# Kernel optimization log

Measured on AMD Instinct MI355X. Metric: run time of the kernel, lower is better.

Reference implementation:

```python
import jax, jax.numpy as jnp
import numpy as np

K = 3
THETA0 = 0.5
THETA1 = 30.0
ALPHA0 = 3.0
BASE = 0.45
ITERS = 20


def unfold(x, k):
    # torch.nn.Unfold(k, stride=1, padding=k//2): [N,C,H,W] -> [N,C,k*k,H*W]
    # kernel positions in row-major (ki,kj) order, zero padding (matches torch)
    p = k // 2
    N, C, H, W = x.shape
    xp = jnp.pad(x, ((0, 0), (0, 0), (p, p), (p, p)))
    patches = jnp.stack([xp[:, :, i:i + H, j:j + W]
                         for i in range(k) for j in range(k)], axis=2)
    return patches.reshape(N, C, k * k, H * W)


def setup_inputs() -> dict:
    key = jax.random.key(0)
    k1, k2, k3 = jax.random.split(key, 3)
    B, C, H, W = 4, 3, 384, 384
    x = jax.random.uniform(k1, (B, 1, H, W), dtype=jnp.float32)
    targets = jax.random.uniform(k2, (B, 1, H, W), dtype=jnp.float32)
    feature_map = jax.random.uniform(k3, (B, C, H, W), dtype=jnp.float32)
    return {"x": x, "targets": targets, "feature_map": feature_map}


def reference(x, targets, feature_map):
    B, C, H, W = feature_map.shape
    HW = H * W

    # ---- precompute pairwise kernel (done in __init__ in torch) ----
    fm = feature_map + 10.0
    ufm = unfold(fm, K)                                  # [B,C,k2,HW]
    ar = np.arange(K * K)
    spatial = jnp.asarray(((ar // K - K // 2) ** 2 +
                           (ar % K - K // 2) ** 2), dtype=jnp.float32)
    color = -jnp.sum((ufm - fm.reshape(B, C, 1, HW)) ** 2, axis=1) / (2.0 * THETA0 ** 2)
    kernel = ALPHA0 * jnp.exp(color - spatial.reshape(1, -1, 1) / (2.0 * THETA1 ** 2))  # [B,k2,HW]

    # ---- forward ----
    xm = x * targets
    xm = (xm > 0.5).astype(x.dtype) * (1.0 - 2.0 * BASE) + BASE
    ret = jnp.concatenate([1.0 - xm, xm], axis=1)        # [B,2,H,W]

    def body(_, r):
        u = unfold(-jnp.log(r), K)                       # [B,2,k2,HW]
        aggre = jnp.sum(u * kernel[:, None], axis=2)     # [B,2,HW]
        f = jnp.exp(-aggre).reshape(B, 2, H, W)
        f = jnp.concatenate([f[:, :1], f[:, 1:] * targets], axis=1)
        f = f + 1e-6
        f = f / jnp.sum(f, axis=1, keepdims=True)
        f = (f > 0.5).astype(f.dtype) * (1.0 - 2.0 * BASE) + BASE
        return f

    ret = jax.lax.fori_loop(0, ITERS, body, ret)

    out = (ret[:, 1:] > 0.5).astype(ret.dtype)           # [B,1,H,W]
    count = jnp.sum(out.reshape(B, -1), axis=1)
    valid = ((count >= HW * 0.05) & (count <= HW * 0.95)).astype(jnp.float32)
    return out, valid
```

## Files before the change

kernel.cpp:

```cpp
#include <hip/hip_runtime.h>
#include <math.h>

namespace {

constexpr int Hh = 384;
constexpr int Ww = 384;
constexpr int Bb = 4;
constexpr int HW = Hh * Ww;
constexpr int NPIX = Bb * HW;
constexpr int ROUNDS = 10;
constexpr int TPB = 256;

constexpr int TILE_W = 64;
constexpr int TILE_H = 8;
constexpr int TX = Ww / TILE_W;
constexpr int TY = Hh / TILE_H;
constexpr int BLKS_PER_B = TX * TY;
constexpr int NBLK = Bb * BLKS_PER_B;

constexpr int H2DW = 20;
constexpr int H2TOT = 12 * H2DW;

constexpr int MIDS = 68;
constexpr int NRING = 148;

constexpr int FMR = 12, FMC = 70, FMPL = FMR * FMC;
constexpr int FMTOT = 3 * FMPL;
constexpr int QR = 11, QC = 68, QPL = QR * QC;
constexpr int QTOT = 4 * QPL;

__device__ __forceinline__ float fsub_rn_(float a, float b) {
    return __fadd_rn(a, -b);
}

__device__ __forceinline__ unsigned ld_agent_u32(const void* p) {
    return __hip_atomic_load((const unsigned*)p, __ATOMIC_RELAXED,
                             __HIP_MEMORY_SCOPE_AGENT);
}
__device__ __forceinline__ void st_agent_u16(void* p, unsigned short v) {
    __hip_atomic_store((unsigned short*)p, v, __ATOMIC_RELAXED,
                       __HIP_MEMORY_SCOPE_AGENT);
}
__device__ __forceinline__ int ld_agent_i32(const int* p) {
    return __hip_atomic_load(p, __ATOMIC_RELAXED, __HIP_MEMORY_SCOPE_AGENT);
}
__device__ __forceinline__ void st_agent_i32(int* p, int v) {
    __hip_atomic_store(p, v, __ATOMIC_RELAXED, __HIP_MEMORY_SCOPE_AGENT);
}

template <int STRIDE>
__device__ __forceinline__ unsigned mf_state(const unsigned char* base,
                                             const float* w9, float tpx,
                                             float Lg45, float Lg55) {
    float a0 = 0.0f, a1 = 0.0f;
#pragma unroll
    for (int ki = 0; ki < 3; ++ki) {
#pragma unroll
        for (int kj = 0; kj < 3; ++kj) {
            const int k = ki * 3 + kj;
            unsigned char s = base[ki * STRIDE + kj];
            float u0 = (s & 1) ? Lg55 : Lg45;
            float u1 = (s & 2) ? Lg55 : Lg45;
            a0 = __fadd_rn(a0, __fmul_rn(u0, w9[k]));
            a1 = __fadd_rn(a1, __fmul_rn(u1, w9[k]));
        }
    }
    float f0 = expf(-a0);
    float f1 = __fmul_rn(expf(-a1), tpx);
    f0 = __fadd_rn(f0, 1e-6f);
    f1 = __fadd_rn(f1, 1e-6f);
    float S = __fadd_rn(f0, f1);
    float f0n = __fdiv_rn(f0, S);
    float f1n = __fdiv_rn(f1, S);
    return (f0n > 0.5f ? 1u : 0u) | (f1n > 0.5f ? 2u : 0u);
}

__device__ __forceinline__ void ring_coords(int ri, int& er, int& ec) {
    if (ri < 66)       { er = 0;        ec = ri; }
    else if (ri < 132) { er = 9;        ec = ri - 66; }
    else if (ri < 140) { er = ri - 131; ec = 0; }
    else               { er = ri - 139; ec = 65; }
}

__global__ __launch_bounds__(TPB, 6) void fused_kernel(
        const float* __restrict__ x, const float* __restrict__ t,
        const float* __restrict__ fm, float* __restrict__ out,
        int* __restrict__ arrive, int* __restrict__ flags,
        int* __restrict__ partial,
        unsigned char* __restrict__ st0, unsigned char* __restrict__ st1) {
    const int tid = threadIdx.x;
    const int bid = blockIdx.x;
    const int b = bid / BLKS_PER_B;
    const int rr_ = bid - b * BLKS_PER_B;
    const int ty = rr_ / TX, tx = rr_ - ty * TX;
    const int row0 = ty * TILE_H, col0 = tx * TILE_W;
    const int tr = tid >> 5;
    const int tc = (tid & 31) * 2;
    const int row = row0 + tr, col = col0 + tc;
    const int hw = row * Ww + col;
    const int gp = b * HW + hw;

    bool nactive = false;
    const int* nflag = nullptr;
    if (tid < 8) {
        const int l2 = (tid < 4) ? tid : tid + 1;
        const int dy = l2 / 3 - 1, dx = l2 - (l2 / 3) * 3 - 1;
        const int nty = ty + dy, ntx = tx + dx;
        if (nty >= 0 && nty < TY && ntx >= 0 && ntx < TX) {
            nactive = true;
            nflag = &flags[(b * BLKS_PER_B + nty * TX + ntx) << 4];
        }
    }

    const float Lg45 = (float)(-log((double)0.45f));
    const float Lg55 = (float)(-log((double)0.55f));

    float2 xv = reinterpret_cast<const float2*>(x)[gp >> 1];
    float2 tv = reinterpret_cast<const float2*>(t)[gp >> 1];
    const float tj[2] = {tv.x, tv.y};
    {
        unsigned short pack =
            (unsigned short)(((__fmul_rn(xv.x, tv.x) > 0.5f) ? 2u : 1u) |
                             (((__fmul_rn(xv.y, tv.y) > 0.5f) ? 2u : 1u) << 8));
        st_agent_u16(st0 + gp, pack);
    }
    __syncthreads();
    if (tid == 0) st_agent_i32(&flags[bid << 4], (1 << 2) | 3);

    __shared__ float pbuf[FMTOT + QTOT];
    float* fmS = pbuf;
    float* wdir = pbuf + FMTOT;
    const float* fmb = fm + (size_t)b * 3 * HW;
    for (int i = tid; i < FMTOT; i += TPB) {
        const int c = i / FMPL, rem = i - c * FMPL;
        const int r = rem / FMC, fc = rem - r * FMC;
        const int ir = min(max(row0 - 2 + r, 0), Hh - 1);
        const int ic = min(max(col0 - 3 + fc, 0), Ww - 1);
        fmS[i] = fmb[c * HW + ir * Ww + ic];
    }
    __syncthreads();

    const float SPK1 = __fdiv_rn(1.0f, 1800.0f);
    const float SPK2 = __fdiv_rn(2.0f, 1800.0f);
    auto wtap = [&](int fr, int fc, float c0, float c1, float c2, float spk) {
        float d0 = fsub_rn_(__fadd_rn(fmS[0 * FMPL + fr * FMC + fc], 10.0f), c0);
        float d1 = fsub_rn_(__fadd_rn(fmS[1 * FMPL + fr * FMC + fc], 10.0f), c1);
        float d2 = fsub_rn_(__fadd_rn(fmS[2 * FMPL + fr * FMC + fc], 10.0f), c2);
        float ss = __fadd_rn(__fadd_rn(__fmul_rn(d0, d0), __fmul_rn(d1, d1)),
                             __fmul_rn(d2, d2));
        float color = __fmul_rn(-ss, 2.0f);
        return __fmul_rn(3.0f, expf(fsub_rn_(color, spk)));
    };
    for (int i = tid; i < QPL; i += TPB) {
        const int qr = i / QC, qcc = i - qr * QC;
        const int ir = row0 - 1 + qr, ic = col0 - 2 + qcc;
        float w0 = 0.0f, w1 = 0.0f, w2 = 0.0f, w3 = 0.0f;
        if (ir >= 0 && ir < Hh && ic >= 0 && ic < Ww) {
            const int fr = qr + 1, fc = qcc + 1;
            float c0 = __fadd_rn(fmS[0 * FMPL + fr * FMC + fc], 10.0f);
            float c1 = __fadd_rn(fmS[1 * FMPL + fr * FMC + fc], 10.0f);
            float c2 = __fadd_rn(fmS[2 * FMPL + fr * FMC + fc], 10.0f);
            const bool up = (ir - 1 >= 0), lf = (ic - 1 >= 0), rg = (ic + 1 < Ww);
            if (up && lf) w0 = wtap(fr - 1, fc - 1, c0, c1, c2, SPK2);
            if (up)       w1 = wtap(fr - 1, fc,     c0, c1, c2, SPK1);
            if (up && rg) w2 = wtap(fr - 1, fc + 1, c0, c1, c2, SPK2);
            if (lf)       w3 = wtap(fr,     fc - 1, c0, c1, c2, SPK1);
        }
        wdir[0 * QPL + i] = w0;
        wdir[1 * QPL + i] = w1;
        wdir[2 * QPL + i] = w2;
        wdir[3 * QPL + i] = w3;
    }
    __syncthreads();

    float wall[2][9];
#pragma unroll
    for (int j = 0; j < 2; ++j) {
        const int qp = (tr + 1) * QC + (tc + j + 2);
        wall[j][0] = wdir[0 * QPL + qp];
        wall[j][1] = wdir[1 * QPL + qp];
        wall[j][2] = wdir[2 * QPL + qp];
        wall[j][3] = wdir[3 * QPL + qp];
        wall[j][4] = 3.0f;
        wall[j][5] = wdir[3 * QPL + qp + 1];
        wall[j][6] = wdir[2 * QPL + qp + QC - 1];
        wall[j][7] = wdir[1 * QPL + qp + QC];
        wall[j][8] = wdir[0 * QPL + qp + QC + 1];
    }
    bool ringv = false;
    int rer = 0, rec = 0;
    float rw[9] = {0, 0, 0, 0, 0, 0, 0, 0, 0};
    float rt = 0.0f;
    if (tid < NRING) {
        ring_coords(tid, rer, rec);
        const int irow = row0 - 1 + rer, icol = col0 - 1 + rec;
        ringv = (irow >= 0 && irow < Hh && icol >= 0 && icol < Ww);
        if (ringv) {
            const int qp = rer * QC + (rec + 1);
            rw[0] = wdir[0 * QPL + qp];
            rw[1] = wdir[1 * QPL + qp];
            rw[2] = wdir[2 * QPL + qp];
            rw[3] = wdir[3 * QPL + qp];
            rw[4] = 3.0f;
            rw[5] = wdir[3 * QPL + qp + 1];
            rw[6] = wdir[2 * QPL + qp + QC - 1];
            rw[7] = wdir[1 * QPL + qp + QC];
            rw[8] = wdir[0 * QPL + qp + QC + 1];
            rt = t[(size_t)b * HW + irow * Ww + icol];
        }
    }

    __shared__ unsigned lds_h2[H2TOT];
    __shared__ unsigned char lds_mid[10 * MIDS];
    __shared__ int sskip;
    __shared__ int schg[4];
    __shared__ int sred[4];

    int pchg = 1;

    for (int r = 0; r < ROUNDS; ++r) {
        const bool fin = (r == ROUNDS - 1);
        const unsigned char* cur = (r & 1) ? st1 : st0;
        unsigned char* nxt = (r & 1) ? st0 : st1;

        if (tid < 64) {
            int nchg = 0;
            for (;;) {
                bool ok = true;
                if (nactive) {
                    int f = ld_agent_i32(nflag);
                    int part = f >> 2;
                    ok = (part >= r + 1);
                    if (ok) nchg = (part == r + 1) ? ((f >> 1) & 1) : (f & 1);
                }
                if (__all(ok)) break;
                __builtin_amdgcn_s_sleep(1);
            }
            bool unch = nactive ? (nchg == 0) : true;
            int au = __all(unch);
            if (tid == 0) sskip = au;
        }
        __syncthreads();
        const bool skip = (r > 0) && (sskip != 0) && (pchg == 0);

        const unsigned char* h2b = (const unsigned char*)lds_h2;
        unsigned n2[2];
        int chg;

        if (skip) {
            n2[0] = h2b[(tr + 2) * 80 + tc + 8];
            n2[1] = h2b[(tr + 2) * 80 + tc + 9];
            chg = 0;
            if (!fin && tid == 0)
                st_agent_i32(&flags[bid << 4], ((r + 2) << 2) | (0 << 1) | pchg);
        } else {
            if (tid < H2TOT) {
                const unsigned char* base2 =
                    cur + (size_t)b * HW + (row0 - 2) * Ww + (col0 - 8);
                const int hr = tid / H2DW, hc = tid - hr * H2DW;
                lds_h2[tid] = ld_agent_u32(base2 + hr * Ww + hc * 4);
            }
            __syncthreads();

#pragma unroll
            for (int j = 0; j < 2; ++j) {
                unsigned m = mf_state<80>(h2b + (tr + 1) * 80 + tc + 7 + j,
                                          wall[j], tj[j], Lg45, Lg55);
                lds_mid[(tr + 1) * MIDS + tc + j + 1] = (unsigned char)m;
            }
            if (ringv) {
                unsigned m = mf_state<80>(h2b + rer * 80 + rec + 6,
                                          rw, rt, Lg45, Lg55);
                lds_mid[rer * MIDS + rec] = (unsigned char)m;
            }
            __syncthreads();

#pragma unroll
            for (int j = 0; j < 2; ++j)
                n2[j] = mf_state<MIDS>(lds_mid + tr * MIDS + tc + j,
                                       wall[j], tj[j], Lg45, Lg55);

            bool diff = (n2[0] != (unsigned)h2b[(tr + 2) * 80 + tc + 8]) ||
                        (n2[1] != (unsigned)h2b[(tr + 2) * 80 + tc + 9]);
            {
                int any = __any(diff);
                if ((tid & 63) == 0) schg[tid >> 6] = any;
            }
            if (!fin)
                st_agent_u16(nxt + gp, (unsigned short)(n2[0] | (n2[1] << 8)));
            __syncthreads();
            chg = (schg[0] | schg[1] | schg[2] | schg[3]) ? 1 : 0;
            if (!fin && tid == 0)
                st_agent_i32(&flags[bid << 4], ((r + 2) << 2) | (chg << 1) | pchg);
        }
        pchg = chg;

        if (fin) {
            const float o0 = (n2[0] & 2) ? 1.0f : 0.0f;
            const float o1 = (n2[1] & 2) ? 1.0f : 0.0f;
            reinterpret_cast<float2*>(out)[gp >> 1] = make_float2(o0, o1);
            int cnt = (o0 != 0.0f) + (o1 != 0.0f);
            const int lane = tid & 63;
            const int wv = tid >> 6;
#pragma unroll
            for (int off = 32; off; off >>= 1) cnt += __shfl_down(cnt, off, 64);
            if (lane == 0) sred[wv] = cnt;
            __syncthreads();
            if (tid == 0) {
                int tot = sred[0] + sred[1] + sred[2] + sred[3];
                st_agent_i32(&partial[bid], tot);
            }
        }
    }

    __syncthreads();
    if (tid == 0)
        __hip_atomic_fetch_add(&arrive[(bid & 15) << 4], 1,
                               __ATOMIC_RELAXED, __HIP_MEMORY_SCOPE_AGENT);
    if (bid == 0) {
        if (tid < 64) {
            for (;;) {
                int v = 0;
                if (tid < 16) v = ld_agent_i32(&arrive[tid << 4]);
#pragma unroll
                for (int off = 1; off < 64; off <<= 1) v += __shfl_xor(v, off, 64);
                if (v >= NBLK) break;
                __builtin_amdgcn_s_sleep(1);
            }
        }
        __syncthreads();
        const int wv = tid >> 6;
        const int lane = tid & 63;
        const int base = wv * BLKS_PER_B;
        int s = 0;
#pragma unroll
        for (int k = 0; k < 4; ++k) s += ld_agent_i32(&partial[base + 64 * k + lane]);
        if (lane < 32) s += ld_agent_i32(&partial[base + 256 + lane]);
#pragma unroll
        for (int off = 32; off; off >>= 1) s += __shfl_down(s, off, 64);
        if (lane == 0) {
            float cf = (float)s;
            const float lo = (float)(147456.0 * 0.05);
            const float hi = (float)(147456.0 * 0.95);
            out[NPIX + wv] = (cf >= lo && cf <= hi) ? 1.0f : 0.0f;
        }
    }
}

}

extern "C" void kernel_launch(void* const* d_in, const int* in_sizes, int n_in,
                              void* d_out, int out_size, void* d_ws, size_t ws_size,
                              hipStream_t stream) {
    const float* x  = (const float*)d_in[0];
    const float* tg = (const float*)d_in[1];
    const float* fm = (const float*)d_in[2];
    float* out = (float*)d_out;

    char* ws = (char*)d_ws;
    int* arrive  = (int*)ws;
    int* flags   = (int*)(ws + 1024);
    int* partial = (int*)(ws + 74752);
    unsigned char* st0 = (unsigned char*)(ws + 81920);
    unsigned char* st1 = st0 + NPIX + 2048;

    (void)hipMemsetAsync(ws, 0, 74752, stream);

    fused_kernel<<<NBLK, TPB, 0, stream>>>(x, tg, fm, out, arrive, flags,
                                           partial, st0, st1);
}
```

Baseline: 52.30 us.

## Add global convergence counter to exit iteration loop early once all blocks stable

Each block that skips a round (no neighbour or own changes) increments a per-round striped global counter. From round 2 on, every block reads the previous round's counter, and if all blocks were unchanged it publishes a terminal flag and breaks out, writing its outputs from the current LDS state. The goal is to stop the remaining rounds of per-block flag polling and barriers once the whole image has converged. The cost is an extra atomic plus a global read and barrier per round, and a larger workspace memset.

```diff
diff --git a/kernel.cpp b/kernel.cpp
--- a/kernel.cpp
+++ b/kernel.cpp
@@ -86,7 +86,7 @@
         const float* __restrict__ x, const float* __restrict__ t,
         const float* __restrict__ fm, float* __restrict__ out,
         int* __restrict__ arrive, int* __restrict__ flags,
-        int* __restrict__ partial,
+        int* __restrict__ conv, int* __restrict__ partial,
         unsigned char* __restrict__ st0, unsigned char* __restrict__ st1) {
     const int tid = threadIdx.x;
     const int bid = blockIdx.x;
@@ -213,15 +213,36 @@
     __shared__ unsigned lds_h2[H2TOT];
     __shared__ unsigned char lds_mid[10 * MIDS];
     __shared__ int sskip;
+    __shared__ int sdone;
     __shared__ int schg[4];
     __shared__ int sred[4];
 
     int pchg = 1;
+    float o0 = 0.0f, o1 = 0.0f;
 
     for (int r = 0; r < ROUNDS; ++r) {
         const bool fin = (r == ROUNDS - 1);
         const unsigned char* cur = (r & 1) ? st1 : st0;
         unsigned char* nxt = (r & 1) ? st0 : st1;
+
+        if (r >= 2) {
+            int v = 0;
+            if (tid < 16) v = ld_agent_i32(&conv[((r - 1) * 16 + tid) << 4]);
+            if (tid < 64) {
+#pragma unroll
+                for (int off = 1; off < 64; off <<= 1) v += __shfl_xor(v, off, 64);
+                if (tid == 0) sdone = (v >= NBLK);
+            }
+            __syncthreads();
+            if (sdone != 0) {
+                if (tid == 0)
+                    st_agent_i32(&flags[bid << 4], (ROUNDS + 2) << 2);
+                const unsigned char* h2b = (const unsigned char*)lds_h2;
+                o0 = (h2b[(tr + 2) * 80 + tc + 8] & 2) ? 1.0f : 0.0f;
+                o1 = (h2b[(tr + 2) * 80 + tc + 9] & 2) ? 1.0f : 0.0f;
+                break;
+            }
+        }
 
         if (tid < 64) {
             int nchg = 0;
@@ -251,8 +272,13 @@
             n2[0] = h2b[(tr + 2) * 80 + tc + 8];
             n2[1] = h2b[(tr + 2) * 80 + tc + 9];
             chg = 0;
-            if (!fin && tid == 0)
-                st_agent_i32(&flags[bid << 4], ((r + 2) << 2) | (0 << 1) | pchg);
+            if (tid == 0) {
+                if (!fin)
+                    st_agent_i32(&flags[bid << 4],
+                                 ((r + 2) << 2) | (0 << 1) | pchg);
+                __hip_atomic_fetch_add(&conv[(r * 16 + (bid & 15)) << 4], 1,
+                                       __ATOMIC_RELAXED, __HIP_MEMORY_SCOPE_AGENT);
+            }
         } else {
             if (tid < H2TOT) {
                 const unsigned char* base2 =
@@ -296,23 +322,25 @@
         pchg = chg;
 
         if (fin) {
-            const float o0 = (n2[0] & 2) ? 1.0f : 0.0f;
-            const float o1 = (n2[1] & 2) ? 1.0f : 0.0f;
-            reinterpret_cast<float2*>(out)[gp >> 1] = make_float2(o0, o1);
-            int cnt = (o0 != 0.0f) + (o1 != 0.0f);
-            const int lane = tid & 63;
-            const int wv = tid >> 6;
-#pragma unroll
-            for (int off = 32; off; off >>= 1) cnt += __shfl_down(cnt, off, 64);
-            if (lane == 0) sred[wv] = cnt;
-            __syncthreads();
-            if (tid == 0) {
-                int tot = sred[0] + sred[1] + sred[2] + sred[3];
-                st_agent_i32(&partial[bid], tot);
-            }
-        }
-    }
-
+            o0 = (n2[0] & 2) ? 1.0f : 0.0f;
+            o1 = (n2[1] & 2) ? 1.0f : 0.0f;
+        }
+    }
+
+    reinterpret_cast<float2*>(out)[gp >> 1] = make_float2(o0, o1);
+    {
+        int cnt = (o0 != 0.0f) + (o1 != 0.0f);
+        const int lane = tid & 63;
+        const int wv = tid >> 6;
+#pragma unroll
+        for (int off = 32; off; off >>= 1) cnt += __shfl_down(cnt, off, 64);
+        if (lane == 0) sred[wv] = cnt;
+    }
+    __syncthreads();
+    if (tid == 0) {
+        int tot = sred[0] + sred[1] + sred[2] + sred[3];
+        st_agent_i32(&partial[bid], tot);
+    }
     __syncthreads();
     if (tid == 0)
         __hip_atomic_fetch_add(&arrive[(bid & 15) << 4], 1,
@@ -360,12 +388,13 @@
     char* ws = (char*)d_ws;
     int* arrive  = (int*)ws;
     int* flags   = (int*)(ws + 1024);
-    int* partial = (int*)(ws + 74752);
-    unsigned char* st0 = (unsigned char*)(ws + 81920);
+    int* conv    = (int*)(ws + 74752);
+    int* partial = (int*)(ws + 84992);
+    unsigned char* st0 = (unsigned char*)(ws + 92160);
     unsigned char* st1 = st0 + NPIX + 2048;
 
-    (void)hipMemsetAsync(ws, 0, 74752, stream);
+    (void)hipMemsetAsync(ws, 0, 84992, stream);
 
     fused_kernel<<<NBLK, TPB, 0, stream>>>(x, tg, fm, out, arrive, flags,
-                                           partial, st0, st1);
-}
+                                           conv, partial, st0, st1);
+}
```

Result: slower. 78.85 us (+50.8%).
